# Kernel tuning notes

Hardware: AMD Instinct MI355X
Metric: run time of the kernel (lower is better)

## Reference

```python
import jax, jax.numpy as jnp
import numpy as np

NC, NG, NP = 8192, 4096, 140
FD, D, L = 512, 256, 2
E_OBS, E_COEXP, E_PPI, E_SYM = 300000, 200000, 10000, 20000
EPS = 1e-5


def layer_norm(x, g, b):
    mu = jnp.mean(x, -1, keepdims=True)
    v = jnp.mean((x - mu) ** 2, -1, keepdims=True)
    return (x - mu) * jax.lax.rsqrt(v + EPS) * g + b


def sage(h_src, h_dst, src, dst, w, Ws, Wn, b, n_dst):
    # DGL SAGEConv (mean aggregator, edge-weighted): mean over incoming
    # weighted messages, then fc_self(h_dst) + fc_neigh(neigh) + bias.
    m = h_src[src] * w[:, None]                                  # [E, D]
    neigh = jax.ops.segment_sum(m, dst, num_segments=n_dst)      # [n_dst, D]
    deg = jax.ops.segment_sum(jnp.ones_like(w), dst, num_segments=n_dst)
    neigh = neigh / jnp.maximum(deg, 1.0)[:, None]
    return h_dst @ Ws + neigh @ Wn + b


def setup_inputs() -> dict:
    key = jax.random.key(0)
    ks = iter(jax.random.split(key, 64))
    def n(*s):
        return jax.random.normal(next(ks), s, jnp.float32) * 0.02
    def u(e):
        return jax.random.uniform(next(ks), (e,), jnp.float32)
    def ri(e, hi):
        return jax.random.randint(next(ks), (e,), 0, hi, jnp.int32)
    return dict(
        cell_feat=jax.random.normal(next(ks), (NC, FD), jnp.float32),
        gene_feat=jax.random.normal(next(ks), (NG, FD), jnp.float32),
        pro_idx=jnp.arange(NP, dtype=jnp.int32),
        obs_src=ri(E_OBS, NG), obs_dst=ri(E_OBS, NC), obs_w=u(E_OBS),
        rev_obs_src=ri(E_OBS, NC), rev_obs_dst=ri(E_OBS, NG), rev_obs_w=u(E_OBS),
        symbol_src=ri(E_SYM, NG), symbol_dst=ri(E_SYM, NP), symbol_w=u(E_SYM),
        rev_symbol_src=ri(E_SYM, NP), rev_symbol_dst=ri(E_SYM, NG), rev_symbol_w=u(E_SYM),
        coexp_src=ri(E_COEXP, NG), coexp_dst=ri(E_COEXP, NG), coexp_w=u(E_COEXP),
        ppi_src=ri(E_PPI, NP), ppi_dst=ri(E_PPI, NP), ppi_w=u(E_PPI),
        W_emb_cell=n(FD, D), b_emb_cell=jnp.zeros((D,), jnp.float32),
        W_emb_gene=n(FD, D), b_emb_gene=jnp.zeros((D,), jnp.float32),
        emb_pro=n(NP, D),
        W_mlpcell=n(L, D, D), b_mlpcell=jnp.zeros((L, D), jnp.float32),
        W_sage_self=n(L, 6, D, D), W_sage_neigh=n(L, 6, D, D),
        b_sage=jnp.zeros((L, 6, D), jnp.float32),
        ln1_g=jnp.ones((L, 3, D), jnp.float32), ln1_b=jnp.zeros((L, 3, D), jnp.float32),
        ln2_g=jnp.ones((L, 3, D), jnp.float32), ln2_b=jnp.zeros((L, 3, D), jnp.float32),
        W_last=n(3 * D, NP), b_last=jnp.zeros((NP,), jnp.float32),
    )


def reference(cell_feat, gene_feat, pro_idx,
              obs_src, obs_dst, obs_w,
              rev_obs_src, rev_obs_dst, rev_obs_w,
              symbol_src, symbol_dst, symbol_w,
              rev_symbol_src, rev_symbol_dst, rev_symbol_w,
              coexp_src, coexp_dst, coexp_w,
              ppi_src, ppi_dst, ppi_w,
              W_emb_cell, b_emb_cell, W_emb_gene, b_emb_gene, emb_pro,
              W_mlpcell, b_mlpcell, W_sage_self, W_sage_neigh, b_sage,
              ln1_g, ln1_b, ln2_g, ln2_b, W_last, b_last):
    act = jax.nn.selu
    hc = cell_feat @ W_emb_cell + b_emb_cell      # emb_cell
    hg = gene_feat @ W_emb_gene + b_emb_gene      # emb_gene
    hp = emb_pro[pro_idx]                         # nn.Embedding path
    nc, ng, npn = hc.shape[0], hg.shape[0], hp.shape[0]
    hist = [hc]
    for l in range(W_mlpcell.shape[0]):
        Ws, Wn, bs = W_sage_self[l], W_sage_neigh[l], b_sage[l]
        hmlp = layer_norm(act(hc @ W_mlpcell[l] + b_mlpcell[l]), ln1_g[l, 2], ln1_b[l, 2])
        # HeteroGraphConv(SAGE) over edges_sub = [obs, rev_obs, symbol, rev_symbol] (stack)
        s_obs = sage(hg, hc, obs_src, obs_dst, obs_w, Ws[0], Wn[0], bs[0], nc)
        s_robs = sage(hc, hg, rev_obs_src, rev_obs_dst, rev_obs_w, Ws[1], Wn[1], bs[1], ng)
        s_sym = sage(hg, hp, symbol_src, symbol_dst, symbol_w, Ws[2], Wn[2], bs[2], npn)
        s_rsym = sage(hp, hg, rev_symbol_src, rev_symbol_dst, rev_symbol_w, Ws[3], Wn[3], bs[3], ng)
        # homogeneous subgraph convs: gene_sage on coexp, pro_sage on ppi
        h_gg = layer_norm(act(sage(hg, hg, coexp_src, coexp_dst, coexp_w, Ws[4], Wn[4], bs[4], ng)), ln1_g[l, 0], ln1_b[l, 0])
        h_pp = layer_norm(act(sage(hp, hp, ppi_src, ppi_dst, ppi_w, Ws[5], Wn[5], bs[5], npn)), ln1_g[l, 1], ln1_b[l, 1])
        # norm each stacked relation output, then agg='sum' over the stack dim
        hgen = layer_norm(act(s_robs), ln1_g[l, 0], ln1_b[l, 0]) + layer_norm(act(s_rsym), ln1_g[l, 0], ln1_b[l, 0]) + h_gg
        hpro = layer_norm(act(s_sym), ln1_g[l, 1], ln1_b[l, 1]) + h_pp
        hcel = layer_norm(act(s_obs), ln1_g[l, 2], ln1_b[l, 2]) + hmlp
        hg = layer_norm(act(hgen), ln2_g[l, 0], ln2_b[l, 0])
        hp = layer_norm(act(hpro), ln2_g[l, 1], ln2_b[l, 1])
        hc = layer_norm(act(hcel), ln2_g[l, 2], ln2_b[l, 2])
        hist.append(hc)
    # mlp_last over concat of per-layer cell reps (sum(dims[1:-1]) -> dims[-1])
    return jnp.concatenate(hist, -1) @ W_last + b_last
```

## Files before the change

### kernel.cpp

```cpp
#include <hip/hip_runtime.h>

typedef unsigned short ushort_t;
typedef unsigned int uint_t;

typedef ushort_t ushortx8 __attribute__((ext_vector_type(8)));
typedef ushort_t ushortx4 __attribute__((ext_vector_type(4)));
typedef __bf16 bf16x8 __attribute__((ext_vector_type(8)));
typedef float f32x4 __attribute__((ext_vector_type(4)));

#define NCC 8192
#define NGG 4096
#define NPP 140
#define LDS_STR 88
#define CEPB 16384

__device__ __forceinline__ float bf2f(ushort_t u) {
    uint_t i = ((uint_t)u) << 16;
    float f;
    __builtin_memcpy(&f, &i, 4);
    return f;
}
__device__ __forceinline__ ushort_t f2bf(float f) {
    uint_t i;
    __builtin_memcpy(&i, &f, 4);
    uint_t r = (i + 0x7FFFu + ((i >> 16) & 1u)) >> 16;
    return (ushort_t)r;
}
__device__ __forceinline__ float scrub(float x) {
    return __builtin_isfinite(x) ? x : 0.f;
}
__device__ __forceinline__ float selu_f(float x) {
    return x > 0.f ? 1.0507009873554805f * x : 1.7580993408473766f * expm1f(x);
}
__device__ __forceinline__ float wsum64(float x) {
    for (int o = 32; o; o >>= 1) x += __shfl_xor(x, o, 64);
    return x;
}

__global__ __launch_bounds__(256) void sc_zero1(int* __restrict__ a, int na) {
    int i = blockIdx.x * 256 + threadIdx.x;
    if (i < na) a[i] = 0;
}

struct CountJob {
    const int* dst;
    const int* src;
    const float* w;
    uint_t* pw;
    ushort_t* rank;
    int E;
    int nbins;
    int* deg;
    int bstart;
};
struct CountBatch {
    CountJob j[6];
};
struct TrJob {
    const float* src;
    ushort_t* dst;
    int K, N, nx, nxy;
    int bstart;
};
struct TrBatch {
    TrJob j[6];
};
struct FillJob {
    const int* dst;
    const uint_t* pw;
    const ushort_t* rank;
    int E;
    const int* offs;
    uint_t* ep;
    int bstart;
};
struct FillBatch {
    FillJob j[6];
};
struct GemmJob {
    const void* A1;
    int lda1, K1, af1;
    const ushort_t* Bt1;
    const ushort_t* A2;
    int K2;
    const ushort_t* Bt2;
    const float* bias;
    ushort_t* C;
    int ldc, M;
    int mstart;
};
struct GemmBatch {
    GemmJob j[7];
};

struct CountArgs {
    CountBatch cb;
    int bsC;
    const float* cf;
    ushort_t* cf16;
    int nbC;
    const float* gf;
    ushort_t* gf16;
};
__global__ __launch_bounds__(1024) void sc_count(CountArgs ca) {
    __shared__ int hist[NCC];
    int bx = blockIdx.x;
    const int tid = threadIdx.x;
    if (bx >= ca.bsC) {
        bx -= ca.bsC;
        const float* src;
        ushort_t* dst;
        if (bx < ca.nbC) {
            src = ca.cf;
            dst = ca.cf16;
        } else {
            bx -= ca.nbC;
            src = ca.gf;
            dst = ca.gf16;
        }
        size_t i = ((size_t)bx * 1024 + tid) * 8;
        float4 f0 = *(const float4*)(src + i);
        float4 f1 = *(const float4*)(src + i + 4);
        ushortx8 v;
        v[0] = f2bf(f0.x);
        v[1] = f2bf(f0.y);
        v[2] = f2bf(f0.z);
        v[3] = f2bf(f0.w);
        v[4] = f2bf(f1.x);
        v[5] = f2bf(f1.y);
        v[6] = f2bf(f1.z);
        v[7] = f2bf(f1.w);
        *(ushortx8*)(dst + i) = v;
        return;
    }
    int r = 0;
#pragma unroll
    for (int i = 1; i < 6; ++i) r = (bx >= ca.cb.j[i].bstart) ? i : r;
    const CountJob& J = ca.cb.j[r];
    const int nb = J.nbins;
    for (int b = tid; b < nb; b += 1024) hist[b] = 0;
    __syncthreads();
    const int e0 = (bx - J.bstart) * CEPB;
    ushort_t lrk[16];
#pragma unroll
    for (int u = 0; u < 16; ++u) {
        int e = e0 + u * 1024 + tid;
        if (e < J.E) {
            int d = J.dst[e];
            lrk[u] = (ushort_t)atomicAdd(&hist[d], 1);
            J.pw[e] = ((uint_t)f2bf(J.w[e]) << 16) | (uint_t)J.src[e];
        }
    }
    __syncthreads();
    for (int b = tid; b < nb; b += 1024) {
        int c = hist[b];
        if (c > 0) hist[b] = atomicAdd(&J.deg[b], c);
    }
    __syncthreads();
#pragma unroll
    for (int u = 0; u < 16; ++u) {
        int e = e0 + u * 1024 + tid;
        if (e < J.E) {
            int d = J.dst[e];
            J.rank[e] = (ushort_t)(hist[d] + (int)lrk[u]);
        }
    }
}

struct PrepArgs {
    TrBatch tb;
    int bsT;
    const float* emb;
    const int* pidx;
    ushort_t* hp;
    int nEmb;
};
__global__ __launch_bounds__(256) void sc_prep(PrepArgs pa) {
    __shared__ ushort_t t[32][33];
    int bx = blockIdx.x;
    if (bx < pa.bsT) {
        int r = 0;
#pragma unroll
        for (int i = 1; i < 6; ++i) r = (bx >= pa.tb.j[i].bstart) ? i : r;
        const TrJob& J = pa.tb.j[r];
        int local = bx - J.bstart;
        int b = local / J.nxy, rem = local % J.nxy;
        int n0 = (rem % J.nx) * 32, k0 = (rem / J.nx) * 32;
        const float* s = J.src + (size_t)b * J.K * J.N;
        ushort_t* d = J.dst + (size_t)b * J.K * J.N;
        int x = threadIdx.x & 31, y = threadIdx.x >> 5;
        for (int i = y; i < 32; i += 8) {
            int k = k0 + i, n = n0 + x;
            t[i][x] = (k < J.K && n < J.N) ? f2bf(s[(size_t)k * J.N + n]) : (ushort_t)0;
        }
        __syncthreads();
        for (int i = y; i < 32; i += 8) {
            int n = n0 + i, k = k0 + x;
            if (n < J.N && k < J.K) d[(size_t)n * J.K + k] = t[x][i];
        }
        return;
    }
    bx -= pa.bsT;
    int i = bx * 256 + threadIdx.x;
    if (i < pa.nEmb) {
        int r = i >> 8, c = i & 255;
        int j = pa.pidx[r];
        j = (uint_t)j < (uint_t)NPP ? j : 0;
        pa.hp[i] = f2bf(pa.emb[(size_t)j * 256 + c]);
    }
}

__global__ __launch_bounds__(1024) void sc_csr_scan6(const int* __restrict__ deg_base,
                                                     int* __restrict__ offs_base) {
    const int ndst[6] = {NCC, NGG, NPP, NGG, NGG, NPP};
    const int dstart[6] = {0, NCC, NCC + NGG, NCC + NGG + NPP, NCC + 2 * NGG + NPP,
                           NCC + 3 * NGG + NPP};
    const int ostart[6] = {0, NCC + 1, NCC + NGG + 2, NCC + NGG + NPP + 3,
                           NCC + 2 * NGG + NPP + 4, NCC + 3 * NGG + NPP + 5};
    int r = blockIdx.x;
    const int* deg = deg_base + dstart[r];
    int* offs = offs_base + ostart[r];
    int n = ndst[r];
    __shared__ int wsum[16];
    __shared__ int carry;
    int tid = threadIdx.x, wave = tid >> 6, lane = tid & 63;
    if (tid == 0) carry = 0;
    __syncthreads();
    for (int base = 0; base < n; base += 1024) {
        int i = base + tid;
        int v = (i < n) ? deg[i] : 0;
        int x = v;
#pragma unroll
        for (int o = 1; o < 64; o <<= 1) {
            int tv = __shfl_up(x, o, 64);
            if (lane >= o) x += tv;
        }
        if (lane == 63) wsum[wave] = x;
        __syncthreads();
        if (tid == 0) {
            int acc = 0;
#pragma unroll
            for (int k = 0; k < 16; ++k) {
                int tv = wsum[k];
                wsum[k] = acc;
                acc += tv;
            }
        }
        __syncthreads();
        int incl = x + wsum[wave];
        int cr = carry;
        if (i < n) offs[i] = cr + incl - v;
        __syncthreads();
        if (tid == 1023) carry = cr + incl;
        __syncthreads();
    }
    if (tid == 0) offs[n] = carry;
}

__device__ __forceinline__ void gemm_body(const GemmBatch& gbat, int mbx, int n0, ushort_t* As,
                                          ushort_t* Bs) {
    int r = 0;
#pragma unroll
    for (int i = 1; i < 7; ++i) r = (mbx >= gbat.j[i].mstart) ? i : r;
    const void* JA1 = gbat.j[r].A1;
    const int lda1 = gbat.j[r].lda1, K1j = gbat.j[r].K1, af1 = gbat.j[r].af1;
    const ushort_t* JBt1 = gbat.j[r].Bt1;
    const ushort_t* JA2 = gbat.j[r].A2;
    const int K2j = gbat.j[r].K2;
    const ushort_t* JBt2 = gbat.j[r].Bt2;
    const float* bias = gbat.j[r].bias;
    ushort_t* C = gbat.j[r].C;
    const int ldc = gbat.j[r].ldc, M = gbat.j[r].M;
    const int tid = threadIdx.x;
    const int wave = tid >> 6, lane = tid & 63;
    const int lr = lane & 15, lq = lane >> 4;
    const int m0 = (mbx - gbat.j[r].mstart) * 128;
    f32x4 acc[2][4] = {};
    for (int pass = 0; pass < 2; ++pass) {
        const void* A = pass ? (const void*)JA2 : JA1;
        const ushort_t* Bt = pass ? JBt2 : JBt1;
        const int K = pass ? K2j : K1j;
        const int lda = pass ? 256 : lda1;
        const int af = pass ? 0 : af1;
        if (K == 0 || A == nullptr) continue;
        for (int k0 = 0; k0 < K; k0 += 64) {
            __syncthreads();
#pragma unroll
            for (int i = 0; i < 4; ++i) {
                int g = tid + i * 256;
                int rr = g >> 3, c = (g & 7) * 8;
                ushortx8 v = {0, 0, 0, 0, 0, 0, 0, 0};
                int gm = m0 + rr;
                if (gm < M) {
                    if (af) {
                        const float* Af = (const float*)A;
                        float4 f0 = *(const float4*)(Af + (size_t)gm * lda + k0 + c);
                        float4 f1 = *(const float4*)(Af + (size_t)gm * lda + k0 + c + 4);
                        v[0] = f2bf(f0.x);
                        v[1] = f2bf(f0.y);
                        v[2] = f2bf(f0.z);
                        v[3] = f2bf(f0.w);
                        v[4] = f2bf(f1.x);
                        v[5] = f2bf(f1.y);
                        v[6] = f2bf(f1.z);
                        v[7] = f2bf(f1.w);
                    } else {
                        v = *(const ushortx8*)((const ushort_t*)A + (size_t)gm * lda + k0 + c);
                    }
                }
                *(ushortx8*)(&As[rr * LDS_STR + c]) = v;
            }
#pragma unroll
            for (int i = 0; i < 2; ++i) {
                int g = tid + i * 256;
                int rr = g >> 3, c = (g & 7) * 8;
                int gn = n0 + rr;
                ushortx8 v = *(const ushortx8*)(Bt + (size_t)gn * K + k0 + c);
                *(ushortx8*)(&Bs[rr * LDS_STR + c]) = v;
            }
            __syncthreads();
#pragma unroll
            for (int kk = 0; kk < 64; kk += 32) {
                bf16x8 a0 = __builtin_bit_cast(
                    bf16x8, *(const ushortx8*)(&As[(wave * 32 + lr) * LDS_STR + kk + lq * 8]));
                bf16x8 a1 = __builtin_bit_cast(
                    bf16x8,
                    *(const ushortx8*)(&As[(wave * 32 + 16 + lr) * LDS_STR + kk + lq * 8]));
                bf16x8 b0 = __builtin_bit_cast(
                    bf16x8, *(const ushortx8*)(&Bs[(lr)*LDS_STR + kk + lq * 8]));
                bf16x8 b1 = __builtin_bit_cast(
                    bf16x8, *(const ushortx8*)(&Bs[(16 + lr) * LDS_STR + kk + lq * 8]));
                bf16x8 b2 = __builtin_bit_cast(
                    bf16x8, *(const ushortx8*)(&Bs[(32 + lr) * LDS_STR + kk + lq * 8]));
                bf16x8 b3 = __builtin_bit_cast(
                    bf16x8, *(const ushortx8*)(&Bs[(48 + lr) * LDS_STR + kk + lq * 8]));
                acc[0][0] = __builtin_amdgcn_mfma_f32_16x16x32_bf16(a0, b0, acc[0][0], 0, 0, 0);
                acc[0][1] = __builtin_amdgcn_mfma_f32_16x16x32_bf16(a0, b1, acc[0][1], 0, 0, 0);
                acc[0][2] = __builtin_amdgcn_mfma_f32_16x16x32_bf16(a0, b2, acc[0][2], 0, 0, 0);
                acc[0][3] = __builtin_amdgcn_mfma_f32_16x16x32_bf16(a0, b3, acc[0][3], 0, 0, 0);
                acc[1][0] = __builtin_amdgcn_mfma_f32_16x16x32_bf16(a1, b0, acc[1][0], 0, 0, 0);
                acc[1][1] = __builtin_amdgcn_mfma_f32_16x16x32_bf16(a1, b1, acc[1][1], 0, 0, 0);
                acc[1][2] = __builtin_amdgcn_mfma_f32_16x16x32_bf16(a1, b2, acc[1][2], 0, 0, 0);
                acc[1][3] = __builtin_amdgcn_mfma_f32_16x16x32_bf16(a1, b3, acc[1][3], 0, 0, 0);
            }
        }
    }
#pragma unroll
    for (int mt = 0; mt < 2; ++mt)
#pragma unroll
        for (int nt = 0; nt < 4; ++nt) {
            int col = n0 + nt * 16 + lr;
            float bb = bias[col];
#pragma unroll
            for (int v = 0; v < 4; ++v) {
                int row = m0 + wave * 32 + mt * 16 + lq * 4 + v;
                if (row >= M) continue;
                C[(size_t)row * ldc + col] = f2bf(scrub(acc[mt][nt][v] + bb));
            }
        }
}

__global__ __launch_bounds__(256) void sc_gemm_batch(GemmBatch gbat) {
    __shared__ __align__(16) ushort_t As[128 * LDS_STR];
    __shared__ __align__(16) ushort_t Bs[64 * LDS_STR];
    gemm_body(gbat, blockIdx.x, blockIdx.y * 64, As, Bs);
}

struct Emb64Job {
    const ushort_t* A;
    const ushort_t* Bt;
    const float* bias;
    ushort_t* C;
    int ldc;
    int mstart;
};
struct FillGemmArgs {
    Emb64Job ej[2];
    int gemmBlocks;
    FillBatch fb;
};
__global__ __launch_bounds__(256) void sc_fill_gemm(FillGemmArgs fg) {
    __shared__ __align__(16) ushort_t As[64 * LDS_STR];
    __shared__ __align__(16) ushort_t Bs[64 * LDS_STR];
    int bx = blockIdx.x;
    if (bx >= fg.gemmBlocks) {
        bx -= fg.gemmBlocks;
        int r = 0;
#pragma unroll
        for (int i = 1; i < 6; ++i) r = (bx >= fg.fb.j[i].bstart) ? i : r;
        const FillJob& J = fg.fb.j[r];
        int e = (bx - J.bstart) * 256 + threadIdx.x;
        if (e < J.E) {
            int d = J.dst[e];
            J.ep[J.offs[d] + (int)J.rank[e]] = J.pw[e];
        }
        return;
    }
    const int mb = bx >> 2, n0 = (bx & 3) * 64;
    const int r = (mb >= fg.ej[1].mstart) ? 1 : 0;
    const Emb64Job& J = fg.ej[r];
    const int m0 = (mb - J.mstart) * 64;
    const ushort_t* A = J.A;
    const ushort_t* Bt = J.Bt;
    const int tid = threadIdx.x;
    const int wave = tid >> 6, lane = tid & 63;
    const int lr = lane & 15, lq = lane >> 4;
    f32x4 acc[4] = {};
    for (int k0 = 0; k0 < 512; k0 += 64) {
        __syncthreads();
#pragma unroll
        for (int i = 0; i < 2; ++i) {
            int g = tid + i * 256;
            int rr = g >> 3, c = (g & 7) * 8;
            *(ushortx8*)(&As[rr * LDS_STR + c]) =
                *(const ushortx8*)(A + (size_t)(m0 + rr) * 512 + k0 + c);
            *(ushortx8*)(&Bs[rr * LDS_STR + c]) =
                *(const ushortx8*)(Bt + (size_t)(n0 + rr) * 512 + k0 + c);
        }
        __syncthreads();
#pragma unroll
        for (int kk = 0; kk < 64; kk += 32) {
            bf16x8 a = __builtin_bit_cast(
                bf16x8, *(const ushortx8*)(&As[(wave * 16 + lr) * LDS_STR + kk + lq * 8]));
            bf16x8 b0 =
                __builtin_bit_cast(bf16x8, *(const ushortx8*)(&Bs[(lr)*LDS_STR + kk + lq * 8]));
            bf16x8 b1 = __builtin_bit_cast(
                bf16x8, *(const ushortx8*)(&Bs[(16 + lr) * LDS_STR + kk + lq * 8]));
            bf16x8 b2 = __builtin_bit_cast(
                bf16x8, *(const ushortx8*)(&Bs[(32 + lr) * LDS_STR + kk + lq * 8]));
            bf16x8 b3 = __builtin_bit_cast(
                bf16x8, *(const ushortx8*)(&Bs[(48 + lr) * LDS_STR + kk + lq * 8]));
            acc[0] = __builtin_amdgcn_mfma_f32_16x16x32_bf16(a, b0, acc[0], 0, 0, 0);
            acc[1] = __builtin_amdgcn_mfma_f32_16x16x32_bf16(a, b1, acc[1], 0, 0, 0);
            acc[2] = __builtin_amdgcn_mfma_f32_16x16x32_bf16(a, b2, acc[2], 0, 0, 0);
            acc[3] = __builtin_amdgcn_mfma_f32_16x16x32_bf16(a, b3, acc[3], 0, 0, 0);
        }
    }
#pragma unroll
    for (int nt = 0; nt < 4; ++nt) {
        int col = n0 + nt * 16 + lr;
        float bb = J.bias[col];
#pragma unroll
        for (int v = 0; v < 4; ++v) {
            int row = m0 + wave * 16 + lq * 4 + v;
            J.C[(size_t)row * J.ldc + col] = f2bf(scrub(acc[nt][v] + bb));
        }
    }
}

struct GatherJob {
    const ushort_t* hsrc;
    int src_ld, src_n;
    const int* offs;
    const uint_t* ep;
    ushort_t* out;
    int row_start;
};
struct GatherBatch {
    GatherJob j[6];
};
__global__ __launch_bounds__(256) void sc_gather_all(GatherBatch gb, int total_rows) {
    int grow = blockIdx.x * 4 + (threadIdx.x >> 6);
    if (grow >= total_rows) return;
    int r = 0;
#pragma unroll
    for (int i = 1; i < 6; ++i) r = (grow >= gb.j[i].row_start) ? i : r;
    r = __builtin_amdgcn_readfirstlane(r);
    const char* hsrc = (const char*)gb.j[r].hsrc;
    const uint_t row_bytes = (uint_t)(gb.j[r].src_ld * 2);
    const uint_t src_n = (uint_t)gb.j[r].src_n;
    const int* offs = gb.j[r].offs;
    const uint_t* ep = gb.j[r].ep;
    ushort_t* out = gb.j[r].out;
    int row = grow - gb.j[r].row_start;
    int lane = threadIdx.x & 63;
    int cb = lane * 8;
    int s0 = offs[row], s1 = offs[row + 1];
    float a0 = 0.f, a1 = 0.f, a2 = 0.f, a3 = 0.f;
    for (int base = s0; base < s1; base += 64) {
        int e = base + lane;
        uint_t myp = (e < s1) ? ep[e] : 0u;
        int cnt = s1 - base;
        cnt = cnt < 64 ? cnt : 64;
        int ng = (cnt + 15) >> 4;
        uint2 bufA[16], bufB[16];
        auto loadg = [&](uint2* buf, int gg) {
#pragma unroll
            for (int u = 0; u < 16; ++u) {
                uint_t pw = (uint_t)__builtin_amdgcn_readlane((int)myp, gg * 16 + u);
                uint_t s = pw & 0xFFFFu;
                s = s < src_n ? s : 0u;
                buf[u] = *(const uint2*)(hsrc + (size_t)(s * row_bytes) + cb);
            }
        };
        auto accg = [&](const uint2* buf, int gg) {
#pragma unroll
            for (int u = 0; u < 16; ++u) {
                uint_t pw = (uint_t)__builtin_amdgcn_readlane((int)myp, gg * 16 + u);
                float w = bf2f((ushort_t)(pw >> 16));
                uint2 v = buf[u];
                uint_t x0 = v.x << 16, x1 = v.x & 0xFFFF0000u;
                uint_t x2 = v.y << 16, x3 = v.y & 0xFFFF0000u;
                a0 = fmaf(w, __builtin_bit_cast(float, x0), a0);
                a1 = fmaf(w, __builtin_bit_cast(float, x1), a1);
                a2 = fmaf(w, __builtin_bit_cast(float, x2), a2);
                a3 = fmaf(w, __builtin_bit_cast(float, x3), a3);
            }
        };
        loadg(bufA, 0);
        int g = 0;
        for (; g + 2 <= ng; g += 2) {
            loadg(bufB, g + 1);
            accg(bufA, g);
            if (g + 2 < ng) loadg(bufA, g + 2);
            accg(bufB, g + 1);
        }
        if (g < ng) accg(bufA, g);
    }
    float inv = 1.f / fmaxf((float)(s1 - s0), 1.f);
    ushort_t* o = out + (size_t)row * 256 + lane * 4;
    o[0] = f2bf(scrub(a0 * inv));
    o[1] = f2bf(scrub(a1 * inv));
    o[2] = f2bf(scrub(a2 * inv));
    o[3] = f2bf(scrub(a3 * inv));
}

__global__ __launch_bounds__(256) void sc_gemm(const ushort_t* __restrict__ A1, int lda1,
                                               const ushort_t* __restrict__ Bt1, int K1,
                                               const float* __restrict__ bias,
                                               float* __restrict__ Cf, int ldc, int M, int N) {
    __shared__ __align__(16) ushort_t As[128 * LDS_STR];
    __shared__ __align__(16) ushort_t Bs[64 * LDS_STR];
    const int tid = threadIdx.x;
    const int wave = tid >> 6, lane = tid & 63;
    const int lr = lane & 15, lq = lane >> 4;
    const int m0 = blockIdx.x * 128, n0 = blockIdx.y * 64;
    f32x4 acc[2][4] = {};
    for (int k0 = 0; k0 < K1; k0 += 64) {
        __syncthreads();
#pragma unroll
        for (int i = 0; i < 4; ++i) {
            int g = tid + i * 256;
            int r = g >> 3, c = (g & 7) * 8;
            ushortx8 v = {0, 0, 0, 0, 0, 0, 0, 0};
            int gm = m0 + r;
            if (gm < M) v = *(const ushortx8*)(A1 + (size_t)gm * lda1 + k0 + c);
            *(ushortx8*)(&As[r * LDS_STR + c]) = v;
        }
#pragma unroll
        for (int i = 0; i < 2; ++i) {
            int g = tid + i * 256;
            int r = g >> 3, c = (g & 7) * 8;
            ushortx8 v = {0, 0, 0, 0, 0, 0, 0, 0};
            int gn = n0 + r;
            if (gn < N) v = *(const ushortx8*)(Bt1 + (size_t)gn * K1 + k0 + c);
            *(ushortx8*)(&Bs[r * LDS_STR + c]) = v;
        }
        __syncthreads();
#pragma unroll
        for (int kk = 0; kk < 64; kk += 32) {
            bf16x8 a0 = __builtin_bit_cast(
                bf16x8, *(const ushortx8*)(&As[(wave * 32 + lr) * LDS_STR + kk + lq * 8]));
            bf16x8 a1 = __builtin_bit_cast(
                bf16x8, *(const ushortx8*)(&As[(wave * 32 + 16 + lr) * LDS_STR + kk + lq * 8]));
            bf16x8 b0 =
                __builtin_bit_cast(bf16x8, *(const ushortx8*)(&Bs[(lr)*LDS_STR + kk + lq * 8]));
            bf16x8 b1 = __builtin_bit_cast(
                bf16x8, *(const ushortx8*)(&Bs[(16 + lr) * LDS_STR + kk + lq * 8]));
            bf16x8 b2 = __builtin_bit_cast(
                bf16x8, *(const ushortx8*)(&Bs[(32 + lr) * LDS_STR + kk + lq * 8]));
            bf16x8 b3 = __builtin_bit_cast(
                bf16x8, *(const ushortx8*)(&Bs[(48 + lr) * LDS_STR + kk + lq * 8]));
            acc[0][0] = __builtin_amdgcn_mfma_f32_16x16x32_bf16(a0, b0, acc[0][0], 0, 0, 0);
            acc[0][1] = __builtin_amdgcn_mfma_f32_16x16x32_bf16(a0, b1, acc[0][1], 0, 0, 0);
            acc[0][2] = __builtin_amdgcn_mfma_f32_16x16x32_bf16(a0, b2, acc[0][2], 0, 0, 0);
            acc[0][3] = __builtin_amdgcn_mfma_f32_16x16x32_bf16(a0, b3, acc[0][3], 0, 0, 0);
            acc[1][0] = __builtin_amdgcn_mfma_f32_16x16x32_bf16(a1, b0, acc[1][0], 0, 0, 0);
            acc[1][1] = __builtin_amdgcn_mfma_f32_16x16x32_bf16(a1, b1, acc[1][1], 0, 0, 0);
            acc[1][2] = __builtin_amdgcn_mfma_f32_16x16x32_bf16(a1, b2, acc[1][2], 0, 0, 0);
            acc[1][3] = __builtin_amdgcn_mfma_f32_16x16x32_bf16(a1, b3, acc[1][3], 0, 0, 0);
        }
    }
#pragma unroll
    for (int mt = 0; mt < 2; ++mt)
#pragma unroll
        for (int nt = 0; nt < 4; ++nt) {
            int col = n0 + nt * 16 + lr;
            if (col >= N) continue;
            float bb = bias ? bias[col] : 0.f;
#pragma unroll
            for (int v = 0; v < 4; ++v) {
                int row = m0 + wave * 32 + mt * 16 + lq * 4 + v;
                if (row >= M) continue;
                Cf[(size_t)row * ldc + col] = scrub(acc[mt][nt][v] + bb);
            }
        }
}

struct LnJob {
    const ushort_t *sA, *sB, *sC;
    const float *g1, *b1, *g2, *b2;
    ushort_t* out;
    int out_ld;
    int row_start;
};
struct LnBatch {
    LnJob j[3];
};
__global__ __launch_bounds__(256) void sc_fuse_ln_all(LnBatch lb, int total_rows) {
    int grow = blockIdx.x * 4 + (threadIdx.x >> 6);
    if (grow >= total_rows) return;
    int r = 0;
#pragma unroll
    for (int i = 1; i < 3; ++i) r = (grow >= lb.j[i].row_start) ? i : r;
    r = __builtin_amdgcn_readfirstlane(r);
    const ushort_t* srcs[3] = {lb.j[r].sA, lb.j[r].sB, lb.j[r].sC};
    const float* g1 = lb.j[r].g1;
    const float* b1 = lb.j[r].b1;
    const float* g2 = lb.j[r].g2;
    const float* b2 = lb.j[r].b2;
    ushort_t* out = lb.j[r].out;
    int out_ld = lb.j[r].out_ld;
    int row = grow - lb.j[r].row_start;
    int lane = threadIdx.x & 63, c = lane * 4;
    float t[4] = {0.f, 0.f, 0.f, 0.f};
#pragma unroll
    for (int si = 0; si < 3; ++si) {
        const ushort_t* s = srcs[si];
        if (!s) continue;
        ushortx4 v = *(const ushortx4*)(s + (size_t)row * 256 + c);
        float x0 = selu_f(scrub(bf2f(v[0]))), x1 = selu_f(scrub(bf2f(v[1])));
        float x2 = selu_f(scrub(bf2f(v[2]))), x3 = selu_f(scrub(bf2f(v[3])));
        float mu = wsum64(x0 + x1 + x2 + x3) * (1.f / 256.f);
        float d0 = x0 - mu, d1 = x1 - mu, d2 = x2 - mu, d3 = x3 - mu;
        float var = wsum64(d0 * d0 + d1 * d1 + d2 * d2 + d3 * d3) * (1.f / 256.f);
        float rr = rsqrtf(var + 1e-5f);
        t[0] += d0 * rr * g1[c + 0] + b1[c + 0];
        t[1] += d1 * rr * g1[c + 1] + b1[c + 1];
        t[2] += d2 * rr * g1[c + 2] + b1[c + 2];
        t[3] += d3 * rr * g1[c + 3] + b1[c + 3];
    }
    float x0 = selu_f(scrub(t[0])), x1 = selu_f(scrub(t[1]));
    float x2 = selu_f(scrub(t[2])), x3 = selu_f(scrub(t[3]));
    float mu = wsum64(x0 + x1 + x2 + x3) * (1.f / 256.f);
    float d0 = x0 - mu, d1 = x1 - mu, d2 = x2 - mu, d3 = x3 - mu;
    float var = wsum64(d0 * d0 + d1 * d1 + d2 * d2 + d3 * d3) * (1.f / 256.f);
    float rr = rsqrtf(var + 1e-5f);
    ushort_t* o = out + (size_t)row * out_ld + c;
    o[0] = f2bf(scrub(d0 * rr * g2[c + 0] + b2[c + 0]));
    o[1] = f2bf(scrub(d1 * rr * g2[c + 1] + b2[c + 1]));
    o[2] = f2bf(scrub(d2 * rr * g2[c + 2] + b2[c + 2]));
    o[3] = f2bf(scrub(d3 * rr * g2[c + 3] + b2[c + 3]));
}

static inline int cdivi(int a, int b) { return (a + b - 1) / b; }

extern "C" void kernel_launch(void* const* d_in, const int* in_sizes, int n_in, void* d_out,
                              int out_size, void* d_ws, size_t ws_size, hipStream_t stream) {
    const float* cell_feat = (const float*)d_in[0];
    const float* gene_feat = (const float*)d_in[1];
    const int* pro_idx = (const int*)d_in[2];
    const int* edge_src[6] = {(const int*)d_in[3],  (const int*)d_in[6],  (const int*)d_in[9],
                              (const int*)d_in[12], (const int*)d_in[15], (const int*)d_in[18]};
    const int* edge_dst[6] = {(const int*)d_in[4],  (const int*)d_in[7],  (const int*)d_in[10],
                              (const int*)d_in[13], (const int*)d_in[16], (const int*)d_in[19]};
    const float* edge_w[6] = {(const float*)d_in[5],  (const float*)d_in[8],
                              (const float*)d_in[11], (const float*)d_in[14],
                              (const float*)d_in[17], (const float*)d_in[20]};
    const float* W_emb_cell = (const float*)d_in[21];
    const float* b_emb_cell = (const float*)d_in[22];
    const float* W_emb_gene = (const float*)d_in[23];
    const float* b_emb_gene = (const float*)d_in[24];
    const float* emb_pro = (const float*)d_in[25];
    const float* W_mlpcell = (const float*)d_in[26];
    const float* b_mlpcell = (const float*)d_in[27];
    const float* W_sage_self = (const float*)d_in[28];
    const float* W_sage_neigh = (const float*)d_in[29];
    const float* b_sage = (const float*)d_in[30];
    const float* ln1_g = (const float*)d_in[31];
    const float* ln1_b = (const float*)d_in[32];
    const float* ln2_g = (const float*)d_in[33];
    const float* ln2_b = (const float*)d_in[34];
    const float* W_last = (const float*)d_in[35];
    const float* b_last = (const float*)d_in[36];

    const int E_obs = in_sizes[3], E_sym = in_sizes[9], E_coexp = in_sizes[15],
              E_ppi = in_sizes[18];
    const int Er[6] = {E_obs, E_obs, E_sym, E_sym, E_coexp, E_ppi};
    const int Nd[6] = {NCC, NGG, NPP, NGG, NGG, NPP};

    char* p = (char*)d_ws;
    auto carve = [&](size_t bytes) -> char* {
        char* r = p;
        p += ((bytes + 255) & ~(size_t)255);
        return r;
    };
    ushort_t* hist = (ushort_t*)carve((size_t)NCC * 768 * 2);
    ushort_t* hg = (ushort_t*)carve((size_t)NGG * 256 * 2);
    ushort_t* hp = (ushort_t*)carve((size_t)NPP * 256 * 2);
    ushort_t* n_obs = (ushort_t*)carve((size_t)NCC * 256 * 2);
    ushort_t* n_robs = (ushort_t*)carve((size_t)NGG * 256 * 2);
    ushort_t* n_sym = (ushort_t*)carve((size_t)NPP * 256 * 2);
    ushort_t* n_rsym = (ushort_t*)carve((size_t)NGG * 256 * 2);
    ushort_t* n_coexp = (ushort_t*)carve((size_t)NGG * 256 * 2);
    ushort_t* n_ppi = (ushort_t*)carve((size_t)NPP * 256 * 2);
    ushort_t* s_obs = (ushort_t*)carve((size_t)NCC * 256 * 2);
    ushort_t* s_robs = (ushort_t*)carve((size_t)NGG * 256 * 2);
    ushort_t* s_sym = (ushort_t*)carve((size_t)NPP * 256 * 2);
    ushort_t* s_rsym = (ushort_t*)carve((size_t)NGG * 256 * 2);
    ushort_t* s_coexp = (ushort_t*)carve((size_t)NGG * 256 * 2);
    ushort_t* s_ppi = (ushort_t*)carve((size_t)NPP * 256 * 2);
    ushort_t* s_mlp = (ushort_t*)carve((size_t)NCC * 256 * 2);
    ushort_t* Wt_emb_cell = (ushort_t*)carve((size_t)512 * 256 * 2);
    ushort_t* Wt_emb_gene = (ushort_t*)carve((size_t)512 * 256 * 2);
    ushort_t* Wt_mlp = (ushort_t*)carve((size_t)2 * 256 * 256 * 2);
    ushort_t* Wt_self = (ushort_t*)carve((size_t)12 * 256 * 256 * 2);
    ushort_t* Wt_neigh = (ushort_t*)carve((size_t)12 * 256 * 256 * 2);
    ushort_t* Wt_last = (ushort_t*)carve((size_t)140 * 768 * 2);
    const int NDTOT = NCC + 3 * NGG + 2 * NPP;
    int* deg_all = (int*)carve((size_t)NDTOT * 4);
    int* offs_all = (int*)carve((size_t)(NDTOT + 6) * 4);
    const int ETOT = 2 * E_obs + 2 * E_sym + E_coexp + E_ppi;
    uint_t* pw_all = (uint_t*)carve((size_t)ETOT * 4);
    ushort_t* rank_all = (ushort_t*)carve((size_t)ETOT * 2);
    uint_t* ep_all = (uint_t*)carve((size_t)ETOT * 4);
    ushort_t* cf16 = s_obs;
    ushort_t* gf16 = s_coexp;
    (void)ws_size;
    (void)n_in;
    (void)out_size;

    const int dS[6] = {0, NCC, NCC + NGG, NCC + NGG + NPP, NCC + 2 * NGG + NPP,
                       NCC + 3 * NGG + NPP};
    const int oS[6] = {0, NCC + 1, NCC + NGG + 2, NCC + NGG + NPP + 3, NCC + 2 * NGG + NPP + 4,
                       NCC + 3 * NGG + NPP + 5};
    int eS[6];
    eS[0] = 0;
    eS[1] = eS[0] + E_obs;
    eS[2] = eS[1] + E_obs;
    eS[3] = eS[2] + E_sym;
    eS[4] = eS[3] + E_sym;
    eS[5] = eS[4] + E_coexp;

    sc_zero1<<<cdivi(NDTOT, 256), 256, 0, stream>>>(deg_all, NDTOT);
    {
        CountArgs ca;
        int bs = 0;
        for (int r = 0; r < 6; ++r) {
            ca.cb.j[r] = {edge_dst[r], edge_src[r], edge_w[r], pw_all + eS[r], rank_all + eS[r],
                          Er[r],       Nd[r],       deg_all + dS[r], bs};
            bs += cdivi(Er[r], CEPB);
        }
        ca.bsC = bs;
        ca.cf = cell_feat;
        ca.cf16 = cf16;
        ca.nbC = (NCC * 512) / 8192;
        ca.gf = gene_feat;
        ca.gf16 = gf16;
        int nbG = (NGG * 512) / 8192;
        sc_count<<<bs + ca.nbC + nbG, 1024, 0, stream>>>(ca);
    }
    {
        PrepArgs pa;
        int bt = 0;
        auto add = [&](int idx, const float* s, ushort_t* d, int B, int K, int N) {
            int nx = cdivi(N, 32), ny = cdivi(K, 32);
            pa.tb.j[idx] = {s, d, K, N, nx, nx * ny, bt};
            bt += B * nx * ny;
        };
        add(0, W_emb_cell, Wt_emb_cell, 1, 512, 256);
        add(1, W_emb_gene, Wt_emb_gene, 1, 512, 256);
        add(2, W_mlpcell, Wt_mlp, 2, 256, 256);
        add(3, W_sage_self, Wt_self, 12, 256, 256);
        add(4, W_sage_neigh, Wt_neigh, 12, 256, 256);
        add(5, W_last, Wt_last, 1, 768, 140);
        pa.bsT = bt;
        pa.emb = emb_pro;
        pa.pidx = pro_idx;
        pa.hp = hp;
        pa.nEmb = NPP * 256;
        int bsE = cdivi(NPP * 256, 256);
        sc_prep<<<pa.bsT + bsE, 256, 0, stream>>>(pa);
    }
    sc_csr_scan6<<<6, 1024, 0, stream>>>(deg_all, offs_all);
    {
        FillGemmArgs fg;
        fg.ej[0] = {cf16, Wt_emb_cell, b_emb_cell, hist, 768, 0};
        fg.ej[1] = {gf16, Wt_emb_gene, b_emb_gene, hg, 256, NCC / 64};
        fg.gemmBlocks = (NCC / 64 + NGG / 64) * 4;
        int bs = 0;
        for (int r = 0; r < 6; ++r) {
            fg.fb.j[r] = {edge_dst[r], pw_all + eS[r], rank_all + eS[r], Er[r], offs_all + oS[r],
                          ep_all + eS[r], bs};
            bs += cdivi(Er[r], 256);
        }
        sc_fill_gemm<<<fg.gemmBlocks + bs, 256, 0, stream>>>(fg);
    }

    for (int l = 0; l < 2; ++l) {
        const ushort_t* hc_l = hist + l * 256;
        {
            GatherBatch gb;
            const ushort_t* hs[6] = {hg, hc_l, hg, hp, hg, hp};
            const int lds[6] = {256, 768, 256, 256, 256, 256};
            const int sn[6] = {NGG, NCC, NGG, NPP, NGG, NPP};
            ushort_t* outs[6] = {n_obs, n_robs, n_sym, n_rsym, n_coexp, n_ppi};
            int rs = 0;
            for (int r = 0; r < 6; ++r) {
                gb.j[r] = {hs[r], lds[r], sn[r], offs_all + oS[r], ep_all + eS[r], outs[r], rs};
                rs += Nd[r];
            }
            sc_gather_all<<<cdivi(rs, 4), 256, 0, stream>>>(gb, rs);
        }
        {
            const size_t WSZ = 65536;
            GemmBatch gbat;
            gbat.j[0] = {hc_l, 768, 256, 0, Wt_mlp + (size_t)l * WSZ, nullptr, 0, nullptr,
                         b_mlpcell + l * 256, s_mlp, 256, NCC, 0};
            const ushort_t* dstf[6] = {hc_l, hg, hp, hg, hg, hp};
            const int dld[6] = {768, 256, 256, 256, 256, 256};
            const ushort_t* nb[6] = {n_obs, n_robs, n_sym, n_rsym, n_coexp, n_ppi};
            ushort_t* so[6] = {s_obs, s_robs, s_sym, s_rsym, s_coexp, s_ppi};
            int ms = cdivi(NCC, 128);
            for (int r = 0; r < 6; ++r) {
                gbat.j[r + 1] = {dstf[r],
                                 dld[r],
                                 256,
                                 0,
                                 Wt_self + (size_t)(l * 6 + r) * WSZ,
                                 nb[r],
                                 256,
                                 Wt_neigh + (size_t)(l * 6 + r) * WSZ,
                                 b_sage + (l * 6 + r) * 256,
                                 so[r],
                                 256,
                                 Nd[r],
                                 ms};
                ms += cdivi(Nd[r], 128);
            }
            sc_gemm_batch<<<dim3(ms, 4), 256, 0, stream>>>(gbat);
        }
        {
            LnBatch lb;
            lb.j[0] = {s_robs, s_rsym, s_coexp, ln1_g + (l * 3 + 0) * 256,
                       ln1_b + (l * 3 + 0) * 256, ln2_g + (l * 3 + 0) * 256,
                       ln2_b + (l * 3 + 0) * 256, hg, 256, 0};
            lb.j[1] = {s_sym, s_ppi, nullptr, ln1_g + (l * 3 + 1) * 256,
                       ln1_b + (l * 3 + 1) * 256, ln2_g + (l * 3 + 1) * 256,
                       ln2_b + (l * 3 + 1) * 256, hp, 256, NGG};
            lb.j[2] = {s_obs, s_mlp, nullptr, ln1_g + (l * 3 + 2) * 256,
                       ln1_b + (l * 3 + 2) * 256, ln2_g + (l * 3 + 2) * 256,
                       ln2_b + (l * 3 + 2) * 256, hist + (l + 1) * 256, 768, NGG + NPP};
            int rs = NGG + NPP + NCC;
            sc_fuse_ln_all<<<cdivi(rs, 4), 256, 0, stream>>>(lb, rs);
        }
    }

    sc_gemm<<<dim3(64, 3), 256, 0, stream>>>(hist, 768, Wt_last, 768, b_last, (float*)d_out, 140,
                                             NCC, 140);
}
```

Baseline: 390.1 us.

## Gather cell features from compact 256-wide copy and simplify gather loop

The embedding GEMM and the layer-0 layernorm now also write the cell representation into a dense 256-column buffer, and the rev_obs gather reads from that buffer instead of the strided 768-wide history array. The aim is better cache-line and TLB locality for the random cell-row gathers. The gather inner loop also drops its manual double-buffered register prefetch in favour of a plain 16-wide unrolled load-and-accumulate. This costs an extra 4 MB workspace buffer, duplicate writes, and possibly less memory-level parallelism in the gather.

Result: no change. 389.7 us (-0.1%).

```diff
diff --git a/kernel.cpp b/kernel.cpp
--- a/kernel.cpp
+++ b/kernel.cpp
@@ -372,6 +372,7 @@
     const float* bias;
     ushort_t* C;
     int ldc;
+    ushort_t* C2;
     int mstart;
 };
 struct FillGemmArgs {
@@ -443,7 +444,9 @@
 #pragma unroll
         for (int v = 0; v < 4; ++v) {
             int row = m0 + wave * 16 + lq * 4 + v;
-            J.C[(size_t)row * J.ldc + col] = f2bf(scrub(acc[nt][v] + bb));
+            ushort_t val = f2bf(scrub(acc[nt][v] + bb));
+            J.C[(size_t)row * J.ldc + col] = val;
+            if (J.C2) J.C2[(size_t)row * 256 + col] = val;
         }
     }
 }
@@ -482,23 +485,15 @@
         uint_t myp = (e < s1) ? ep[e] : 0u;
         int cnt = s1 - base;
         cnt = cnt < 64 ? cnt : 64;
-        int ng = (cnt + 15) >> 4;
-        uint2 bufA[16], bufB[16];
-        auto loadg = [&](uint2* buf, int gg) {
+        int cnt16 = (cnt + 15) & ~15;
+        for (int jj = 0; jj < cnt16; jj += 16) {
 #pragma unroll
             for (int u = 0; u < 16; ++u) {
-                uint_t pw = (uint_t)__builtin_amdgcn_readlane((int)myp, gg * 16 + u);
+                uint_t pw = (uint_t)__builtin_amdgcn_readlane((int)myp, jj + u);
                 uint_t s = pw & 0xFFFFu;
                 s = s < src_n ? s : 0u;
-                buf[u] = *(const uint2*)(hsrc + (size_t)(s * row_bytes) + cb);
-            }
-        };
-        auto accg = [&](const uint2* buf, int gg) {
-#pragma unroll
-            for (int u = 0; u < 16; ++u) {
-                uint_t pw = (uint_t)__builtin_amdgcn_readlane((int)myp, gg * 16 + u);
                 float w = bf2f((ushort_t)(pw >> 16));
-                uint2 v = buf[u];
+                const uint2 v = *(const uint2*)(hsrc + (size_t)(s * row_bytes) + cb);
                 uint_t x0 = v.x << 16, x1 = v.x & 0xFFFF0000u;
                 uint_t x2 = v.y << 16, x3 = v.y & 0xFFFF0000u;
                 a0 = fmaf(w, __builtin_bit_cast(float, x0), a0);
@@ -506,16 +501,7 @@
                 a2 = fmaf(w, __builtin_bit_cast(float, x2), a2);
                 a3 = fmaf(w, __builtin_bit_cast(float, x3), a3);
             }
-        };
-        loadg(bufA, 0);
-        int g = 0;
-        for (; g + 2 <= ng; g += 2) {
-            loadg(bufB, g + 1);
-            accg(bufA, g);
-            if (g + 2 < ng) loadg(bufA, g + 2);
-            accg(bufB, g + 1);
-        }
-        if (g < ng) accg(bufA, g);
+        }
     }
     float inv = 1.f / fmaxf((float)(s1 - s0), 1.f);
     ushort_t* o = out + (size_t)row * 256 + lane * 4;
@@ -602,6 +588,7 @@
     const float *g1, *b1, *g2, *b2;
     ushort_t* out;
     int out_ld;
+    ushort_t* out2;
     int row_start;
 };
 struct LnBatch {
@@ -621,6 +608,7 @@
     const float* b2 = lb.j[r].b2;
     ushort_t* out = lb.j[r].out;
     int out_ld = lb.j[r].out_ld;
+    ushort_t* out2 = lb.j[r].out2;
     int row = grow - lb.j[r].row_start;
     int lane = threadIdx.x & 63, c = lane * 4;
     float t[4] = {0.f, 0.f, 0.f, 0.f};
@@ -646,11 +634,22 @@
     float d0 = x0 - mu, d1 = x1 - mu, d2 = x2 - mu, d3 = x3 - mu;
     float var = wsum64(d0 * d0 + d1 * d1 + d2 * d2 + d3 * d3) * (1.f / 256.f);
     float rr = rsqrtf(var + 1e-5f);
+    ushort_t o0 = f2bf(scrub(d0 * rr * g2[c + 0] + b2[c + 0]));
+    ushort_t o1 = f2bf(scrub(d1 * rr * g2[c + 1] + b2[c + 1]));
+    ushort_t o2v = f2bf(scrub(d2 * rr * g2[c + 2] + b2[c + 2]));
+    ushort_t o3 = f2bf(scrub(d3 * rr * g2[c + 3] + b2[c + 3]));
     ushort_t* o = out + (size_t)row * out_ld + c;
-    o[0] = f2bf(scrub(d0 * rr * g2[c + 0] + b2[c + 0]));
-    o[1] = f2bf(scrub(d1 * rr * g2[c + 1] + b2[c + 1]));
-    o[2] = f2bf(scrub(d2 * rr * g2[c + 2] + b2[c + 2]));
-    o[3] = f2bf(scrub(d3 * rr * g2[c + 3] + b2[c + 3]));
+    o[0] = o0;
+    o[1] = o1;
+    o[2] = o2v;
+    o[3] = o3;
+    if (out2) {
+        ushort_t* q = out2 + (size_t)row * 256 + c;
+        q[0] = o0;
+        q[1] = o1;
+        q[2] = o2v;
+        q[3] = o3;
+    }
 }
 
 static inline int cdivi(int a, int b) { return (a + b - 1) / b; }
@@ -724,6 +723,7 @@
     uint_t* pw_all = (uint_t*)carve((size_t)ETOT * 4);
     ushort_t* rank_all = (ushort_t*)carve((size_t)ETOT * 2);
     uint_t* ep_all = (uint_t*)carve((size_t)ETOT * 4);
+    ushort_t* hc_cmp = (ushort_t*)carve((size_t)NCC * 256 * 2);
     ushort_t* cf16 = s_obs;
     ushort_t* gf16 = s_coexp;
     (void)ws_size;
@@ -785,8 +785,8 @@
     sc_csr_scan6<<<6, 1024, 0, stream>>>(deg_all, offs_all);
     {
         FillGemmArgs fg;
-        fg.ej[0] = {cf16, Wt_emb_cell, b_emb_cell, hist, 768, 0};
-        fg.ej[1] = {gf16, Wt_emb_gene, b_emb_gene, hg, 256, NCC / 64};
+        fg.ej[0] = {cf16, Wt_emb_cell, b_emb_cell, hist, 768, hc_cmp, 0};
+        fg.ej[1] = {gf16, Wt_emb_gene, b_emb_gene, hg, 256, nullptr, NCC / 64};
         fg.gemmBlocks = (NCC / 64 + NGG / 64) * 4;
         int bs = 0;
         for (int r = 0; r < 6; ++r) {
@@ -801,8 +801,8 @@
         const ushort_t* hc_l = hist + l * 256;
         {
             GatherBatch gb;
-            const ushort_t* hs[6] = {hg, hc_l, hg, hp, hg, hp};
-            const int lds[6] = {256, 768, 256, 256, 256, 256};
+            const ushort_t* hs[6] = {hg, hc_cmp, hg, hp, hg, hp};
+            const int lds[6] = {256, 256, 256, 256, 256, 256};
             const int sn[6] = {NGG, NCC, NGG, NPP, NGG, NPP};
             ushort_t* outs[6] = {n_obs, n_robs, n_sym, n_rsym, n_coexp, n_ppi};
             int rs = 0;
@@ -844,13 +844,14 @@
             LnBatch lb;
             lb.j[0] = {s_robs, s_rsym, s_coexp, ln1_g + (l * 3 + 0) * 256,
                        ln1_b + (l * 3 + 0) * 256, ln2_g + (l * 3 + 0) * 256,
-                       ln2_b + (l * 3 + 0) * 256, hg, 256, 0};
+                       ln2_b + (l * 3 + 0) * 256, hg, 256, nullptr, 0};
             lb.j[1] = {s_sym, s_ppi, nullptr, ln1_g + (l * 3 + 1) * 256,
                        ln1_b + (l * 3 + 1) * 256, ln2_g + (l * 3 + 1) * 256,
-                       ln2_b + (l * 3 + 1) * 256, hp, 256, NGG};
+                       ln2_b + (l * 3 + 1) * 256, hp, 256, nullptr, NGG};
             lb.j[2] = {s_obs, s_mlp, nullptr, ln1_g + (l * 3 + 2) * 256,
                        ln1_b + (l * 3 + 2) * 256, ln2_g + (l * 3 + 2) * 256,
-                       ln2_b + (l * 3 + 2) * 256, hist + (l + 1) * 256, 768, NGG + NPP};
+                       ln2_b + (l * 3 + 2) * 256, hist + (l + 1) * 256, 768,
+                       (l == 0) ? hc_cmp : nullptr, NGG + NPP};
             int rs = NGG + NPP + NCC;
             sc_fuse_ln_all<<<cdivi(rs, 4), 256, 0, stream>>>(lb, rs);
         }
```
